# Performance work log

Measured on AMD Instinct MI355X. Metric: run time of the kernel, lower is better.

## Reference

```python
import jax, jax.numpy as jnp
import numpy as np

NTOKEN, NINP, NCLASS = 50000, 256, 16
B, L = 32, 2048
INITRANGE = 0.1


def setup_inputs() -> dict:
    key = jax.random.key(0)
    k1, k2, k3 = jax.random.split(key, 3)
    inp = jax.random.randint(k1, (B, L), 0, NTOKEN).astype(jnp.int64) if jax.config.jax_enable_x64 else jax.random.randint(k1, (B, L), 0, NTOKEN)
    mask = jnp.ones((B, L), dtype=jnp.float32)
    enc_w = jax.random.uniform(k2, (NTOKEN + 1, NINP), jnp.float32, -INITRANGE, INITRANGE)
    dec_w = jax.random.uniform(k3, (NCLASS, NINP), jnp.float32, -INITRANGE, INITRANGE)
    return {"input": inp, "mask": mask, "enc_w": enc_w, "dec_w": dec_w}


def reference(input, mask, enc_w, dec_w):
    # emb: [B, L, D], masked embedding gather
    emb = enc_w[input] * mask[:, :, None]
    # scores_l = emb_l . sum_k emb_k  ==  (emb @ emb^T).sum(axis=2)
    emb_sum = emb.sum(axis=1)                         # [B, D]
    scores = jnp.einsum('bld,bd->bl', emb, emb_sum)   # [B, L]
    y = jnp.exp(scores) * mask                        # faithful: no max-subtract
    attn = y / y.sum(axis=1, keepdims=True)           # [B, L]
    output = jnp.einsum('bld,bl->bd', emb, attn)      # weighted-sum pooling
    # residual mean pooling
    lens = mask.sum(axis=1, keepdims=True)            # [B, 1]
    avg = emb_sum / lens
    out = output + avg
    return out @ dec_w.T                              # [B, NCLASS]
```

## Files before the change

kernel.cpp:

```cpp
#include <hip/hip_runtime.h>
#include <math.h>

#define BB 32
#define LL 2048
#define DD 256
#define NC 16
#define TPB 256
#define TPR 1024

#define SPLIT 32
#define NBLK  (BB * SPLIT)
#define TOK_CHUNK (LL / SPLIT)
#define TOK_WAVE  (TOK_CHUNK / 4)


__global__ __launch_bounds__(TPB) void kA_partial(
    const int* __restrict__ idx, const float* __restrict__ mask,
    const float4* __restrict__ enc4,
    float* __restrict__ pes, float* __restrict__ plen) {
  const int b     = blockIdx.x / SPLIT;
  const int chunk = blockIdx.x % SPLIT;
  const int wave  = threadIdx.x >> 6;
  const int lane  = threadIdx.x & 63;
  const int tid   = threadIdx.x;
  const int l0 = chunk * TOK_CHUNK + wave * TOK_WAVE;

  int   id_r[TOK_WAVE];
  float m_r[TOK_WAVE];
  #pragma unroll
  for (int t = 0; t < TOK_WAVE; ++t) {
    id_r[t] = idx[b * LL + l0 + t];
    m_r[t]  = mask[b * LL + l0 + t];
  }
  float4 v_r[TOK_WAVE];
  #pragma unroll
  for (int t = 0; t < TOK_WAVE; ++t)
    v_r[t] = enc4[(size_t)id_r[t] * (DD / 4) + lane];

  float4 acc = {0.f, 0.f, 0.f, 0.f};
  float lenacc = 0.f;
  #pragma unroll
  for (int t = 0; t < TOK_WAVE; ++t) {
    const float m = m_r[t];
    acc.x += v_r[t].x * m; acc.y += v_r[t].y * m;
    acc.z += v_r[t].z * m; acc.w += v_r[t].w * m;
    lenacc += m;
  }

  __shared__ float lds[4][DD];
  __shared__ float llds[4];
  lds[wave][lane * 4 + 0] = acc.x;
  lds[wave][lane * 4 + 1] = acc.y;
  lds[wave][lane * 4 + 2] = acc.z;
  lds[wave][lane * 4 + 3] = acc.w;
  if (lane == 0) llds[wave] = lenacc;
  __syncthreads();

  const float s = lds[0][tid] + lds[1][tid] + lds[2][tid] + lds[3][tid];
  pes[(b * SPLIT + chunk) * DD + tid] = s;
  if (tid == 0) plen[b * SPLIT + chunk] = llds[0] + llds[1] + llds[2] + llds[3];
}

__global__ __launch_bounds__(TPR) void kR1(
    const float* __restrict__ pes, const float* __restrict__ plen,
    float* __restrict__ emb_sum, float* __restrict__ lens) {
  const int b   = blockIdx.x;
  const int tid = threadIdx.x;
  const int q   = tid >> 8;
  const int d   = tid & 255;

  float s = 0.f;
  #pragma unroll
  for (int c = q * 8; c < q * 8 + 8; ++c)
    s += pes[(b * SPLIT + c) * DD + d];

  __shared__ float red[4][DD];
  red[q][d] = s;

  float lv = 0.f;
  if (tid < 64) {
    lv = (tid < SPLIT) ? plen[b * SPLIT + tid] : 0.f;
    #pragma unroll
    for (int off = 32; off > 0; off >>= 1) lv += __shfl_xor(lv, off);
    if (tid == 0) lens[b] = lv;
  }
  __syncthreads();
  if (q == 0) emb_sum[b * DD + d] = red[0][d] + red[1][d] + red[2][d] + red[3][d];
}

__global__ __launch_bounds__(TPB) void kB_partial(
    const int* __restrict__ idx, const float* __restrict__ mask,
    const float4* __restrict__ enc4, const float* __restrict__ emb_sum,
    float* __restrict__ pout, float* __restrict__ pys) {
  const int b     = blockIdx.x / SPLIT;
  const int chunk = blockIdx.x % SPLIT;
  const int wave  = threadIdx.x >> 6;
  const int lane  = threadIdx.x & 63;
  const int tid   = threadIdx.x;
  const int l0 = chunk * TOK_CHUNK + wave * TOK_WAVE;

  __shared__ __align__(16) float esb[DD];
  esb[tid] = emb_sum[b * DD + tid];
  __syncthreads();
  const float4 es = *reinterpret_cast<const float4*>(&esb[lane * 4]);

  int   id_r[TOK_WAVE];
  float m_r[TOK_WAVE];
  #pragma unroll
  for (int t = 0; t < TOK_WAVE; ++t) {
    id_r[t] = idx[b * LL + l0 + t];
    m_r[t]  = mask[b * LL + l0 + t];
  }
  float4 v_r[TOK_WAVE];
  #pragma unroll
  for (int t = 0; t < TOK_WAVE; ++t)
    v_r[t] = enc4[(size_t)id_r[t] * (DD / 4) + lane];

  float4 acc = {0.f, 0.f, 0.f, 0.f};
  float ys = 0.f;
  #pragma unroll
  for (int t = 0; t < TOK_WAVE; ++t) {
    const float m = m_r[t];
    const float4 v = v_r[t];
    float d = v.x * es.x + v.y * es.y + v.z * es.z + v.w * es.w;
    #pragma unroll
    for (int off = 32; off > 0; off >>= 1) d += __shfl_xor(d, off);
    const float score = d * m;
    const float y = expf(score) * m;
    const float ym = y * m;
    acc.x += ym * v.x; acc.y += ym * v.y;
    acc.z += ym * v.z; acc.w += ym * v.w;
    ys += y;
  }

  __shared__ float lds[4][DD];
  __shared__ float ylds[4];
  lds[wave][lane * 4 + 0] = acc.x;
  lds[wave][lane * 4 + 1] = acc.y;
  lds[wave][lane * 4 + 2] = acc.z;
  lds[wave][lane * 4 + 3] = acc.w;
  if (lane == 0) ylds[wave] = ys;
  __syncthreads();

  const float s = lds[0][tid] + lds[1][tid] + lds[2][tid] + lds[3][tid];
  pout[(b * SPLIT + chunk) * DD + tid] = s;
  if (tid == 0) pys[b * SPLIT + chunk] = ylds[0] + ylds[1] + ylds[2] + ylds[3];
}

__global__ __launch_bounds__(TPR) void kR2head(
    const float* __restrict__ pout, const float* __restrict__ pys,
    const float* __restrict__ emb_sum, const float* __restrict__ lens,
    const float* __restrict__ dec_w, float* __restrict__ out) {
  const int b   = blockIdx.x;
  const int tid = threadIdx.x;
  const int q   = tid >> 8;
  const int d   = tid & 255;

  float s = 0.f;
  #pragma unroll
  for (int c = q * 8; c < q * 8 + 8; ++c)
    s += pout[(b * SPLIT + c) * DD + d];

  __shared__ float red[4][DD];
  __shared__ __align__(16) float vec[DD];
  __shared__ float ysum_s;
  red[q][d] = s;

  if (tid < 64) {
    float v = (tid < SPLIT) ? pys[b * SPLIT + tid] : 0.f;
    #pragma unroll
    for (int off = 32; off > 0; off >>= 1) v += __shfl_xor(v, off);
    if (tid == 0) ysum_s = v;
  }
  __syncthreads();

  if (q == 0) {
    const float os = red[0][d] + red[1][d] + red[2][d] + red[3][d];
    vec[d] = os / ysum_s + emb_sum[b * DD + d] / lens[b];
  }
  __syncthreads();

  const int wave = tid >> 6;
  const int lane = tid & 63;
  const float4 vv = *reinterpret_cast<const float4*>(&vec[lane * 4]);
  const float4 dw = reinterpret_cast<const float4*>(dec_w)[wave * (DD / 4) + lane];
  float dsum = vv.x * dw.x + vv.y * dw.y + vv.z * dw.z + vv.w * dw.w;
  #pragma unroll
  for (int off = 32; off > 0; off >>= 1) dsum += __shfl_xor(dsum, off);
  if (lane == 0) out[b * NC + wave] = dsum;
}

extern "C" void kernel_launch(void* const* d_in, const int* in_sizes, int n_in,
                              void* d_out, int out_size, void* d_ws, size_t ws_size,
                              hipStream_t stream) {
  const int*    idx   = (const int*)d_in[0];
  const float*  mask  = (const float*)d_in[1];
  const float4* enc4  = (const float4*)d_in[2];
  const float*  dec_w = (const float*)d_in[3];
  float* out = (float*)d_out;

  float* ws = (float*)d_ws;
  float* pes     = ws;
  float* plen    = pes + BB * SPLIT * DD;
  float* pout    = plen + BB * SPLIT;
  float* pys     = pout + BB * SPLIT * DD;
  float* emb_sum = pys + BB * SPLIT;
  float* lens    = emb_sum + BB * DD;

  hipLaunchKernelGGL(kA_partial, dim3(NBLK), dim3(TPB), 0, stream,
                     idx, mask, enc4, pes, plen);
  hipLaunchKernelGGL(kR1, dim3(BB), dim3(TPR), 0, stream, pes, plen, emb_sum, lens);
  hipLaunchKernelGGL(kB_partial, dim3(NBLK), dim3(TPB), 0, stream,
                     idx, mask, enc4, emb_sum, pout, pys);
  hipLaunchKernelGGL(kR2head, dim3(BB), dim3(TPR), 0, stream,
                     pout, pys, emb_sum, lens, dec_w, out);
}
```

Baseline: 31.68 us.

## Materialize masked gathered embeddings in workspace and stream them in second pass

The first pass now writes the masked gathered embedding rows to a contiguous workspace buffer of size B*L*D floats. The attention pass reads that buffer sequentially instead of gathering rows from the embedding table a second time by token index. This swaps a random-access gather for coalesced contiguous reads. The cost is an extra 64 MB write in the first pass plus a 64 MB read, so total memory traffic goes up. Mask handling is folded into the stored values, which keeps the math equivalent.

```diff
diff --git a/kernel.cpp b/kernel.cpp
--- a/kernel.cpp
+++ b/kernel.cpp
@@ -16,7 +16,7 @@
 
 __global__ __launch_bounds__(TPB) void kA_partial(
     const int* __restrict__ idx, const float* __restrict__ mask,
-    const float4* __restrict__ enc4,
+    const float4* __restrict__ enc4, float4* __restrict__ emb4,
     float* __restrict__ pes, float* __restrict__ plen) {
   const int b     = blockIdx.x / SPLIT;
   const int chunk = blockIdx.x % SPLIT;
@@ -42,8 +42,11 @@
   #pragma unroll
   for (int t = 0; t < TOK_WAVE; ++t) {
     const float m = m_r[t];
-    acc.x += v_r[t].x * m; acc.y += v_r[t].y * m;
-    acc.z += v_r[t].z * m; acc.w += v_r[t].w * m;
+    float4 w;
+    w.x = v_r[t].x * m; w.y = v_r[t].y * m;
+    w.z = v_r[t].z * m; w.w = v_r[t].w * m;
+    emb4[(size_t)(b * LL + l0 + t) * (DD / 4) + lane] = w;
+    acc.x += w.x; acc.y += w.y; acc.z += w.z; acc.w += w.w;
     lenacc += m;
   }
 
@@ -77,9 +80,8 @@
   __shared__ float red[4][DD];
   red[q][d] = s;
 
-  float lv = 0.f;
   if (tid < 64) {
-    lv = (tid < SPLIT) ? plen[b * SPLIT + tid] : 0.f;
+    float lv = (tid < SPLIT) ? plen[b * SPLIT + tid] : 0.f;
     #pragma unroll
     for (int off = 32; off > 0; off >>= 1) lv += __shfl_xor(lv, off);
     if (tid == 0) lens[b] = lv;
@@ -88,9 +90,9 @@
   if (q == 0) emb_sum[b * DD + d] = red[0][d] + red[1][d] + red[2][d] + red[3][d];
 }
 
-__global__ __launch_bounds__(TPB) void kB_partial(
-    const int* __restrict__ idx, const float* __restrict__ mask,
-    const float4* __restrict__ enc4, const float* __restrict__ emb_sum,
+__global__ __launch_bounds__(TPB) void kB_seq(
+    const float* __restrict__ mask, const float4* __restrict__ emb4,
+    const float* __restrict__ emb_sum,
     float* __restrict__ pout, float* __restrict__ pys) {
   const int b     = blockIdx.x / SPLIT;
   const int chunk = blockIdx.x % SPLIT;
@@ -104,32 +106,28 @@
   __syncthreads();
   const float4 es = *reinterpret_cast<const float4*>(&esb[lane * 4]);
 
-  int   id_r[TOK_WAVE];
   float m_r[TOK_WAVE];
   #pragma unroll
-  for (int t = 0; t < TOK_WAVE; ++t) {
-    id_r[t] = idx[b * LL + l0 + t];
-    m_r[t]  = mask[b * LL + l0 + t];
-  }
+  for (int t = 0; t < TOK_WAVE; ++t)
+    m_r[t] = mask[b * LL + l0 + t];
+
+  const float4* erow = emb4 + (size_t)(b * LL + l0) * (DD / 4);
   float4 v_r[TOK_WAVE];
   #pragma unroll
   for (int t = 0; t < TOK_WAVE; ++t)
-    v_r[t] = enc4[(size_t)id_r[t] * (DD / 4) + lane];
+    v_r[t] = erow[(size_t)t * (DD / 4) + lane];
 
   float4 acc = {0.f, 0.f, 0.f, 0.f};
   float ys = 0.f;
   #pragma unroll
   for (int t = 0; t < TOK_WAVE; ++t) {
-    const float m = m_r[t];
-    const float4 v = v_r[t];
-    float d = v.x * es.x + v.y * es.y + v.z * es.z + v.w * es.w;
+    const float4 w = v_r[t];
+    float d = w.x * es.x + w.y * es.y + w.z * es.z + w.w * es.w;
     #pragma unroll
     for (int off = 32; off > 0; off >>= 1) d += __shfl_xor(d, off);
-    const float score = d * m;
-    const float y = expf(score) * m;
-    const float ym = y * m;
-    acc.x += ym * v.x; acc.y += ym * v.y;
-    acc.z += ym * v.z; acc.w += ym * v.w;
+    const float y = expf(d) * m_r[t];
+    acc.x += y * w.x; acc.y += y * w.y;
+    acc.z += y * w.z; acc.w += y * w.w;
     ys += y;
   }
 
@@ -200,7 +198,8 @@
   float* out = (float*)d_out;
 
   float* ws = (float*)d_ws;
-  float* pes     = ws;
+  float* emb     = ws;
+  float* pes     = emb + (size_t)BB * LL * DD;
   float* plen    = pes + BB * SPLIT * DD;
   float* pout    = plen + BB * SPLIT;
   float* pys     = pout + BB * SPLIT * DD;
@@ -208,10 +207,10 @@
   float* lens    = emb_sum + BB * DD;
 
   hipLaunchKernelGGL(kA_partial, dim3(NBLK), dim3(TPB), 0, stream,
-                     idx, mask, enc4, pes, plen);
+                     idx, mask, enc4, (float4*)emb, pes, plen);
   hipLaunchKernelGGL(kR1, dim3(BB), dim3(TPR), 0, stream, pes, plen, emb_sum, lens);
-  hipLaunchKernelGGL(kB_partial, dim3(NBLK), dim3(TPB), 0, stream,
-                     idx, mask, enc4, emb_sum, pout, pys);
+  hipLaunchKernelGGL(kB_seq, dim3(NBLK), dim3(TPB), 0, stream,
+                     mask, (const float4*)emb, emb_sum, pout, pys);
   hipLaunchKernelGGL(kR2head, dim3(BB), dim3(TPR), 0, stream,
                      pout, pys, emb_sum, lens, dec_w, out);
 }
```

After: 43.36 us. +36.9%, slower.
